# Optimization experiments

Hardware: AMD Instinct MI355X
Metric: run time of the kernel (lower is better)

Reference implementation:

```python
import jax, jax.numpy as jnp
import numpy as np

DIM = 1024
DEPTH = 8
HEADS = 16
DIM_HEAD = 64
INNER = HEADS * DIM_HEAD  # 1024
NQ = 64
EMB = 768
OUT = 1024
FF_INNER = 4 * DIM
B, N1 = 32, 257
EPS = 1e-5


def layer_norm(x, g, b):
    m = jnp.mean(x, axis=-1, keepdims=True)
    v = jnp.mean(jnp.square(x - m), axis=-1, keepdims=True)
    return (x - m) * jax.lax.rsqrt(v + EPS) * g + b


def split_heads(t):
    # (b, l, inner) -> (b, h, l, dh)
    b, l, _ = t.shape
    return t.reshape(b, l, HEADS, DIM_HEAD).transpose(0, 2, 1, 3)


def setup_inputs() -> dict:
    key = jax.random.key(0)
    ks = jax.random.split(key, 12)
    s = 0.02
    inp = {
        "x": jax.random.normal(ks[0], (B, N1, EMB), jnp.float32),
        "latents": jax.random.normal(ks[1], (1, NQ, DIM), jnp.float32) / np.sqrt(DIM),
        "proj_in_w": jax.random.normal(ks[2], (EMB, DIM), jnp.float32) * s,
        "proj_in_b": jnp.zeros((DIM,), jnp.float32),
        "ln1_g": jnp.ones((DEPTH, DIM), jnp.float32),
        "ln1_b": jnp.zeros((DEPTH, DIM), jnp.float32),
        "ln2_g": jnp.ones((DEPTH, DIM), jnp.float32),
        "ln2_b": jnp.zeros((DEPTH, DIM), jnp.float32),
        "Wq": jax.random.normal(ks[3], (DEPTH, DIM, INNER), jnp.float32) * s,
        "Wkv": jax.random.normal(ks[4], (DEPTH, DIM, 2 * INNER), jnp.float32) * s,
        "Wo": jax.random.normal(ks[5], (DEPTH, INNER, DIM), jnp.float32) * s,
        "ff_ln_g": jnp.ones((DEPTH, DIM), jnp.float32),
        "ff_ln_b": jnp.zeros((DEPTH, DIM), jnp.float32),
        "ff_w1": jax.random.normal(ks[6], (DEPTH, DIM, FF_INNER), jnp.float32) * s,
        "ff_w2": jax.random.normal(ks[7], (DEPTH, FF_INNER, DIM), jnp.float32) * s,
        "proj_out_w": jax.random.uniform(ks[8], (DIM, OUT), jnp.float32, -0.01, 0.01),
        "proj_out_b": jnp.zeros((OUT,), jnp.float32),
        "norm_out_g": jnp.ones((OUT,), jnp.float32),
        "norm_out_b": jnp.zeros((OUT,), jnp.float32),
    }
    return inp


def reference(x, latents, proj_in_w, proj_in_b, ln1_g, ln1_b, ln2_g, ln2_b,
              Wq, Wkv, Wo, ff_ln_g, ff_ln_b, ff_w1, ff_w2,
              proj_out_w, proj_out_b, norm_out_g, norm_out_b):
    # proj_in
    xf = x @ proj_in_w + proj_in_b              # (b, n1, dim)
    lat = jnp.broadcast_to(latents, (x.shape[0], NQ, DIM))
    scale = DIM_HEAD ** -0.25                   # 1/sqrt(sqrt(dim_head))

    for i in range(DEPTH):
        # PerceiverAttention
        xn = layer_norm(xf, ln1_g[i], ln1_b[i])
        ln_lat = layer_norm(lat, ln2_g[i], ln2_b[i])
        q = split_heads(ln_lat @ Wq[i])                       # (b,h,nq,dh)
        kv = jnp.concatenate([xn, ln_lat], axis=1) @ Wkv[i]   # (b,n1+nq,2*inner)
        k, v = jnp.split(kv, 2, axis=-1)
        k, v = split_heads(k), split_heads(v)                 # (b,h,nk,dh)
        w = jnp.einsum('bhqd,bhkd->bhqk', q * scale, k * scale)
        w = jax.nn.softmax(w.astype(jnp.float32), axis=-1).astype(q.dtype)
        o = jnp.einsum('bhqk,bhkd->bhqd', w, v)               # (b,h,nq,dh)
        o = o.transpose(0, 2, 1, 3).reshape(lat.shape[0], NQ, INNER)
        lat = o @ Wo[i] + lat
        # FeedForward: LN -> Linear -> GELU -> Linear
        h = layer_norm(lat, ff_ln_g[i], ff_ln_b[i])
        h = jax.nn.gelu(h @ ff_w1[i], approximate=False) @ ff_w2[i]
        lat = h + lat

    out = lat @ proj_out_w + proj_out_b
    return layer_norm(out, norm_out_g, norm_out_b)
```

## Files before the change

### kernel.cpp

```cpp
#include <hip/hip_runtime.h>
#include <hip/hip_bf16.h>
#include <cstdint>

typedef __hip_bfloat16 bf16;
typedef __attribute__((ext_vector_type(8))) short short8;
typedef __attribute__((ext_vector_type(4))) float f32x4;

__device__ __forceinline__ f32x4 mfma16(short8 a, short8 b, f32x4 c) {
  return __builtin_amdgcn_mfma_f32_16x16x32_bf16(a, b, c, 0, 0, 0);
}

__device__ __forceinline__ void gload16(const bf16* g, bf16* l) {
  __builtin_amdgcn_global_load_lds((const __attribute__((address_space(1))) void*)g,
                                   (__attribute__((address_space(3))) void*)l, 16, 0, 0);
}


__global__ void __launch_bounds__(256) cvt_f32_bf16(const float* __restrict__ in,
                                                    bf16* __restrict__ out, int n) {
  int i = blockIdx.x * 256 + threadIdx.x;
  if (i < n) out[i] = __float2bfloat16(in[i]);
}


__device__ __forceinline__ void trans_tile(float (*tile)[33], const float* __restrict__ src,
                                           bf16* __restrict__ dst, int K, int N,
                                           int bx, int by) {
  int n0 = bx * 32, k0 = by * 32;
  int tx = threadIdx.x & 31, ty = threadIdx.x >> 5;
#pragma unroll
  for (int j = 0; j < 32; j += 8)
    tile[ty + j][tx] = src[(size_t)(k0 + ty + j) * N + n0 + tx];
  __syncthreads();
#pragma unroll
  for (int j = 0; j < 32; j += 8)
    dst[(size_t)(n0 + ty + j) * K + k0 + tx] = __float2bfloat16(tile[tx][ty + j]);
}

__global__ void __launch_bounds__(256) transpose_cvt(const float* __restrict__ src,
                                                     bf16* __restrict__ dst,
                                                     int K, int N) {
  __shared__ float tile[32][33];
  trans_tile(tile, src, dst, K, N, blockIdx.x, blockIdx.y);
}

__global__ void __launch_bounds__(256) transpose_all(
    const float* __restrict__ wq, const float* __restrict__ wkv,
    const float* __restrict__ wo, const float* __restrict__ w1,
    const float* __restrict__ w2, bf16* __restrict__ wq_t, bf16* __restrict__ wkv_t,
    bf16* __restrict__ wo_t, bf16* __restrict__ w1_t, bf16* __restrict__ w2_t) {
  __shared__ float tile[32][33];
  int id = blockIdx.x;
  if (id < 1024) {
    trans_tile(tile, wq, wq_t, 1024, 1024, id & 31, id >> 5);
  } else if (id < 3072) {
    id -= 1024;
    trans_tile(tile, wkv, wkv_t, 1024, 2048, id & 63, id >> 6);
  } else if (id < 4096) {
    id -= 3072;
    trans_tile(tile, wo, wo_t, 1024, 1024, id & 31, id >> 5);
  } else if (id < 8192) {
    id -= 4096;
    trans_tile(tile, w1, w1_t, 1024, 4096, id & 127, id >> 7);
  } else {
    id -= 8192;
    trans_tile(tile, w2, w2_t, 4096, 1024, id & 31, id >> 5);
  }
}


__device__ __forceinline__ void stats_of(const float v[4], int tid, float& mean,
                                         float& rstd, float* red) {
  float s = 0.f, s2 = 0.f;
#pragma unroll
  for (int j = 0; j < 4; j++) { s += v[j]; s2 += v[j] * v[j]; }
#pragma unroll
  for (int o = 32; o > 0; o >>= 1) {
    s += __shfl_down(s, o);
    s2 += __shfl_down(s2, o);
  }
  int w = tid >> 6;
  if ((tid & 63) == 0) { red[w] = s; red[4 + w] = s2; }
  __syncthreads();
  s = red[0] + red[1] + red[2] + red[3];
  s2 = red[4] + red[5] + red[6] + red[7];
  mean = s * (1.f / 1024.f);
  float var = s2 * (1.f / 1024.f) - mean * mean;
  rstd = rsqrtf(var + 1e-5f);
}

__device__ __forceinline__ void row_stats(const float* x, int tid, float v[4],
                                          float& mean, float& rstd, float* red) {
#pragma unroll
  for (int j = 0; j < 4; j++) v[j] = x[tid + j * 256];
  stats_of(v, tid, mean, rstd, red);
}

__global__ void __launch_bounds__(256) ln_to_bf16(const float* __restrict__ in,
                                                  const float* __restrict__ g,
                                                  const float* __restrict__ bb,
                                                  bf16* __restrict__ out) {
  __shared__ float red[8];
  int row = blockIdx.x, tid = threadIdx.x;
  const float* x = in + (size_t)row * 1024;
  float v[4], mean, rstd;
  row_stats(x, tid, v, mean, rstd, red);
  bf16* o1 = out + (size_t)row * 1024;
#pragma unroll
  for (int j = 0; j < 4; j++) {
    int c = tid + j * 256;
    float y = (v[j] - mean) * rstd;
    if (g) y = y * g[c] + bb[c];
    o1[c] = __float2bfloat16(y);
  }
}

template <int LM>
__global__ void __launch_bounds__(256) lncat(const bf16* __restrict__ xhat,
                                             const float* __restrict__ lin,
                                             const float* __restrict__ parts,
                                             const float* __restrict__ lat2,
                                             float* __restrict__ lat,
                                             const float* __restrict__ g1,
                                             const float* __restrict__ b1,
                                             const float* __restrict__ g2,
                                             const float* __restrict__ b2,
                                             bf16* __restrict__ cat,
                                             bf16* __restrict__ lnlat) {
  __shared__ float red[8];
  int row = blockIdx.x, tid = threadIdx.x;
  int bidx = row / 336, n = row - bidx * 336;
  bf16* out = cat + (size_t)row * 1024;
  const size_t MN = (size_t)2048 * 1024;
  if (n < 257) {
    const bf16* in = xhat + ((size_t)bidx * 257 + n) * 1024;
#pragma unroll
    for (int j = 0; j < 4; j++) {
      int c = tid + j * 256;
      out[c] = __float2bfloat16(__bfloat162float(in[c]) * g1[c] + b1[c]);
    }
  } else if (n < 321) {
    int lrow = bidx * 64 + (n - 257);
    float v[4];
#pragma unroll
    for (int j = 0; j < 4; j++) {
      int c = tid + j * 256;
      size_t idx = (size_t)lrow * 1024 + c;
      float a;
      if (LM == 0) {
        a = lin[(size_t)(n - 257) * 1024 + c];
      } else {
        a = parts[idx] + parts[MN + idx] + parts[2 * MN + idx] + parts[3 * MN + idx]
          + lat2[idx];
      }
      lat[idx] = a;
      v[j] = a;
    }
    float mean, rstd;
    stats_of(v, tid, mean, rstd, red);
    bf16* o2 = lnlat + (size_t)lrow * 1024;
#pragma unroll
    for (int j = 0; j < 4; j++) {
      int c = tid + j * 256;
      bf16 hh = __float2bfloat16((v[j] - mean) * rstd * g2[c] + b2[c]);
      out[c] = hh;
      o2[c] = hh;
    }
  } else {
#pragma unroll
    for (int j = 0; j < 4; j++)
      out[tid + j * 256] = __float2bfloat16(0.f);
  }
}


enum { MB_BIAS = 1, MB_RESID = 2, MB_GELU = 4, MB_BF16 = 8 };

template <int MODE>
__device__ __forceinline__ void gemm_tile(
    const bf16* __restrict__ A, const bf16* __restrict__ Bt, void* __restrict__ Cout,
    const float* __restrict__ bias, const float* __restrict__ resid,
    int M, int N, int K, int m0, int n0, int kBeg, int kEnd, size_t planeOff,
    bf16* sA, bf16* sB) {
  int tid = threadIdx.x;
  int wave = tid >> 6, lane = tid & 63;
  int quad = lane >> 4, l16 = lane & 15;
  int wm = (wave >> 1) * 64, wn = (wave & 1) * 64;

  int srow = wave * 16 + (lane >> 2);
  int scol = (lane & 3) * 8;
  const bf16* gA0 = A + (size_t)min(m0 + srow, M - 1) * K + scol;
  const bf16* gA1 = A + (size_t)min(m0 + 64 + srow, M - 1) * K + scol;
  const bf16* gB0 = Bt + (size_t)(n0 + srow) * K + scol;
  const bf16* gB1 = Bt + (size_t)(n0 + 64 + srow) * K + scol;
  bf16* lA0 = &sA[(wave * 16) * 32];
  bf16* lA1 = &sA[(64 + wave * 16) * 32];
  bf16* lB0 = &sB[(wave * 16) * 32];
  bf16* lB1 = &sB[(64 + wave * 16) * 32];

  f32x4 acc[4][4] = {};

  for (int k0 = kBeg; k0 < kEnd; k0 += 32) {
    gload16(gA0 + k0, lA0);
    gload16(gA1 + k0, lA1);
    gload16(gB0 + k0, lB0);
    gload16(gB1 + k0, lB1);
    __syncthreads();
    short8 af[4], bfv[4];
#pragma unroll
    for (int i = 0; i < 4; i++)
      af[i] = *(const short8*)&sA[(wm + i * 16 + l16) * 32 + quad * 8];
#pragma unroll
    for (int j = 0; j < 4; j++)
      bfv[j] = *(const short8*)&sB[(wn + j * 16 + l16) * 32 + quad * 8];
#pragma unroll
    for (int i = 0; i < 4; i++)
#pragma unroll
      for (int j = 0; j < 4; j++)
        acc[i][j] = mfma16(af[i], bfv[j], acc[i][j]);
    __syncthreads();
  }

  float* cf = (float*)Cout + planeOff;
#pragma unroll
  for (int i = 0; i < 4; i++) {
    int grb = m0 + wm + i * 16 + quad * 4;
#pragma unroll
    for (int j = 0; j < 4; j++) {
      int gc = n0 + wn + j * 16 + l16;
      float bv = (MODE & MB_BIAS) ? bias[gc] : 0.f;
#pragma unroll
      for (int r = 0; r < 4; r++) {
        int gr = grb + r;
        if (gr < M) {
          float vv = acc[i][j][r] + bv;
          if (MODE & MB_GELU) vv = 0.5f * vv * (1.f + erff(vv * 0.70710678118654752f));
          if (MODE & MB_RESID) vv += resid[(size_t)gr * N + gc];
          if (MODE & MB_BF16) ((bf16*)Cout)[(size_t)gr * N + gc] = __float2bfloat16(vv);
          else cf[(size_t)gr * N + gc] = vv;
        }
      }
    }
  }
}

template <int MODE>
__global__ void __launch_bounds__(256, 2) gemm_bt(
    const bf16* __restrict__ A, const bf16* __restrict__ Bt,
    void* __restrict__ Cout, const float* __restrict__ bias,
    const float* __restrict__ resid, int M, int N, int K) {
  __shared__ bf16 sA[128 * 32];
  __shared__ bf16 sB[128 * 32];
  int kPer = K / gridDim.z;
  gemm_tile<MODE>(A, Bt, Cout, bias, resid, M, N, K,
                  blockIdx.y * 128, blockIdx.x * 128,
                  blockIdx.z * kPer, (blockIdx.z + 1) * kPer,
                  (size_t)blockIdx.z * ((size_t)M * N), sA, sB);
}

__global__ void __launch_bounds__(256, 2) gemm_qkv(
    const bf16* __restrict__ catb, const bf16* __restrict__ wkv,
    bf16* __restrict__ kvbuf, const bf16* __restrict__ lnlat,
    const bf16* __restrict__ wq, bf16* __restrict__ qbuf) {
  __shared__ bf16 sA[128 * 32];
  __shared__ bf16 sB[128 * 32];
  int by = blockIdx.y, bx = blockIdx.x;
  if (by < 84) {
    gemm_tile<MB_BF16>(catb, wkv, kvbuf, nullptr, nullptr, 10752, 2048, 1024,
                       by * 128, bx * 128, 0, 1024, 0, sA, sB);
  } else {
    int t = (by - 84) * 16 + bx;
    gemm_tile<MB_BF16>(lnlat, wq, qbuf, nullptr, nullptr, 2048, 1024, 1024,
                       (t >> 3) * 128, (t & 7) * 128, 0, 1024, 0, sA, sB);
  }
}


enum { RD_BIAS = 1, RD_RESID = 2, RD_BF16 = 4 };

template <int MODE>
__global__ void __launch_bounds__(256) reduce_k(const float* __restrict__ parts, int S,
                                                int MN, int N,
                                                const float* __restrict__ bias,
                                                const float* __restrict__ resid,
                                                void* __restrict__ out) {
  int i4 = (blockIdx.x * 256 + threadIdx.x) * 4;
  if (i4 >= MN) return;
  float4 a = *(const float4*)&parts[i4];
#pragma unroll 4
  for (int s = 1; s < S; s++) {
    float4 b = *(const float4*)&parts[(size_t)s * MN + i4];
    a.x += b.x; a.y += b.y; a.z += b.z; a.w += b.w;
  }
  if (MODE & RD_BIAS) {
    float4 b = *(const float4*)&bias[i4 & (N - 1)];
    a.x += b.x; a.y += b.y; a.z += b.z; a.w += b.w;
  }
  if (MODE & RD_RESID) {
    float4 b = *(const float4*)&resid[i4];
    a.x += b.x; a.y += b.y; a.z += b.z; a.w += b.w;
  }
  if (MODE & RD_BF16) {
    bf16 o[4] = {__float2bfloat16(a.x), __float2bfloat16(a.y),
                 __float2bfloat16(a.z), __float2bfloat16(a.w)};
    *(uint2*)&((bf16*)out)[i4] = *(uint2*)o;
  } else {
    *(float4*)&((float*)out)[i4] = a;
  }
}

__global__ void __launch_bounds__(256) reduce_ln_resid(
    const float* __restrict__ parts, const float* __restrict__ resid,
    const float* __restrict__ g, const float* __restrict__ bb,
    float* __restrict__ lat2, bf16* __restrict__ lnff) {
  __shared__ float red[8];
  int row = blockIdx.x, tid = threadIdx.x;
  const size_t MN = (size_t)2048 * 1024;
  float v[4];
#pragma unroll
  for (int j = 0; j < 4; j++) {
    int c = tid + j * 256;
    size_t idx = (size_t)row * 1024 + c;
    float a = parts[idx] + parts[MN + idx] + parts[2 * MN + idx] + parts[3 * MN + idx]
            + resid[idx];
    lat2[idx] = a;
    v[j] = a;
  }
  float mean, rstd;
  stats_of(v, tid, mean, rstd, red);
  bf16* o = lnff + (size_t)row * 1024;
#pragma unroll
  for (int j = 0; j < 4; j++) {
    int c = tid + j * 256;
    o[c] = __float2bfloat16((v[j] - mean) * rstd * g[c] + bb[c]);
  }
}

__global__ void __launch_bounds__(256) reduce_bias_ln(
    const float* __restrict__ parts, const float* __restrict__ bias,
    const float* __restrict__ g, const float* __restrict__ bb,
    float* __restrict__ out) {
  __shared__ float red[8];
  int row = blockIdx.x, tid = threadIdx.x;
  const size_t MN = (size_t)2048 * 1024;
  float v[4];
#pragma unroll
  for (int j = 0; j < 4; j++) {
    int c = tid + j * 256;
    size_t idx = (size_t)row * 1024 + c;
    v[j] = parts[idx] + parts[MN + idx] + parts[2 * MN + idx] + parts[3 * MN + idx]
         + bias[c];
  }
  float mean, rstd;
  stats_of(v, tid, mean, rstd, red);
  float* o = out + (size_t)row * 1024;
#pragma unroll
  for (int j = 0; j < 4; j++) {
    int c = tid + j * 256;
    o[c] = (v[j] - mean) * rstd * g[c] + bb[c];
  }
}


__device__ __forceinline__ int swz64(int row, int cb) {
  return (row << 7) + (cb ^ ((row & 7) << 4) ^ (((row >> 3) & 3) << 5));
}

__global__ void __launch_bounds__(256, 2) attn(const bf16* __restrict__ qb,
                                               const bf16* __restrict__ kvb,
                                               bf16* __restrict__ ob) {
  __shared__ bf16 sQ[64 * 64];
  __shared__ bf16 sKV[64 * 64];
  __shared__ bf16 sP[64 * 376];
  __shared__ float sRed[256];
  char* cQ = (char*)sQ;
  char* cKV = (char*)sKV;

  int h = blockIdx.x, b = blockIdx.y;
  int tid = threadIdx.x, wave = tid >> 6, lane = tid & 63;
  int quad = lane >> 4, l16 = lane & 15;

  const bf16* qg = qb + (size_t)b * 64 * 1024 + h * 64;
  const bf16* kg = kvb + (size_t)b * 336 * 2048 + h * 64;
  const bf16* vg = kg + 1024;

  {
    int r = tid >> 3, cb = (tid & 7) * 16;
    *(uint4*)(cQ + swz64(r, cb)) =
        *(const uint4*)((const char*)qg + (size_t)r * 2048 + cb);
    *(uint4*)(cQ + swz64(r + 32, cb)) =
        *(const uint4*)((const char*)qg + (size_t)(r + 32) * 2048 + cb);
  }

  f32x4 accS[6][4] = {};

  for (int g = 0; g < 6; g++) {
    __syncthreads();
    {
      int r = tid >> 3, cb = (tid & 7) * 16;
      int gr = g * 64 + r;
      if (gr < 336)
        *(uint4*)(cKV + swz64(r, cb)) =
            *(const uint4*)((const char*)kg + (size_t)gr * 4096 + cb);
      gr += 32;
      if (gr < 336)
        *(uint4*)(cKV + swz64(r + 32, cb)) =
            *(const uint4*)((const char*)kg + (size_t)gr * 4096 + cb);
    }
    __syncthreads();
    if (g * 4 + wave < 21) {
#pragma unroll
      for (int ks = 0; ks < 2; ks++) {
        short8 bfr = *(const short8*)(cKV + swz64(wave * 16 + l16, ks * 64 + quad * 16));
#pragma unroll
        for (int i = 0; i < 4; i++) {
          short8 afr = *(const short8*)(cQ + swz64(i * 16 + l16, ks * 64 + quad * 16));
          accS[g][i] = mfma16(afr, bfr, accS[g][i]);
        }
      }
    }
  }

  float rmax[4][4], rsum[4][4];
#pragma unroll
  for (int i = 0; i < 4; i++)
#pragma unroll
    for (int r = 0; r < 4; r++) { rmax[i][r] = -1e30f; rsum[i][r] = 0.f; }

#pragma unroll
  for (int g = 0; g < 6; g++) {
    int col = (g * 4 + wave) * 16 + l16;
    bool valid = col < 321;
#pragma unroll
    for (int i = 0; i < 4; i++)
#pragma unroll
      for (int r = 0; r < 4; r++) {
        float v = accS[g][i][r] * 0.125f;
        accS[g][i][r] = v;
        if (valid) rmax[i][r] = fmaxf(rmax[i][r], v);
      }
  }
#pragma unroll
  for (int off = 1; off < 16; off <<= 1)
#pragma unroll
    for (int i = 0; i < 4; i++)
#pragma unroll
      for (int r = 0; r < 4; r++)
        rmax[i][r] = fmaxf(rmax[i][r], __shfl_xor(rmax[i][r], off));
  if (l16 == 0) {
#pragma unroll
    for (int i = 0; i < 4; i++)
#pragma unroll
      for (int r = 0; r < 4; r++)
        sRed[wave * 64 + i * 16 + quad * 4 + r] = rmax[i][r];
  }
  __syncthreads();
#pragma unroll
  for (int i = 0; i < 4; i++)
#pragma unroll
    for (int r = 0; r < 4; r++) {
      int row = i * 16 + quad * 4 + r;
      rmax[i][r] = fmaxf(fmaxf(sRed[row], sRed[64 + row]),
                         fmaxf(sRed[128 + row], sRed[192 + row]));
    }
  __syncthreads();

#pragma unroll
  for (int g = 0; g < 6; g++) {
    int col = (g * 4 + wave) * 16 + l16;
    bool valid = col < 321;
#pragma unroll
    for (int i = 0; i < 4; i++)
#pragma unroll
      for (int r = 0; r < 4; r++) {
        float pv = valid ? __expf(accS[g][i][r] - rmax[i][r]) : 0.f;
        rsum[i][r] += pv;
        if (col < 352) sP[(i * 16 + quad * 4 + r) * 376 + col] = __float2bfloat16(pv);
      }
  }
#pragma unroll
  for (int off = 1; off < 16; off <<= 1)
#pragma unroll
    for (int i = 0; i < 4; i++)
#pragma unroll
      for (int r = 0; r < 4; r++)
        rsum[i][r] += __shfl_xor(rsum[i][r], off);
  if (l16 == 0) {
#pragma unroll
    for (int i = 0; i < 4; i++)
#pragma unroll
      for (int r = 0; r < 4; r++)
        sRed[wave * 64 + i * 16 + quad * 4 + r] = rsum[i][r];
  }
  __syncthreads();
#pragma unroll
  for (int i = 0; i < 4; i++)
#pragma unroll
    for (int r = 0; r < 4; r++) {
      int row = i * 16 + quad * 4 + r;
      rsum[i][r] = sRed[row] + sRed[64 + row] + sRed[128 + row] + sRed[192 + row];
    }

  f32x4 accO[4] = {};
  for (int cch = 0; cch < 6; cch++) {
    __syncthreads();
    {
      int r = tid >> 3, cb = (tid & 7) * 16;
      int gr = cch * 64 + r;
      if (gr < 336)
        *(uint4*)(cKV + swz64(r, cb)) =
            *(const uint4*)((const char*)vg + (size_t)gr * 4096 + cb);
      gr += 32;
      if (gr < 336)
        *(uint4*)(cKV + swz64(r + 32, cb)) =
            *(const uint4*)((const char*)vg + (size_t)gr * 4096 + cb);
    }
    __syncthreads();
    int nks = (cch == 5) ? 1 : 2;
    for (int ks = 0; ks < nks; ks++) {
      short8 bv;
      int cb = (wave * 16 + l16) * 2;
#pragma unroll
      for (int jj = 0; jj < 8; jj++)
        bv[jj] = *(const short*)(cKV + swz64(ks * 32 + quad * 8 + jj, cb));
#pragma unroll
      for (int i = 0; i < 4; i++) {
        short8 ap = *(const short8*)&sP[(i * 16 + l16) * 376 + cch * 64 + ks * 32 + quad * 8];
        accO[i] = mfma16(ap, bv, accO[i]);
      }
    }
  }

#pragma unroll
  for (int i = 0; i < 4; i++)
#pragma unroll
    for (int r = 0; r < 4; r++) {
      int row = i * 16 + quad * 4 + r;
      ob[(size_t)(b * 64 + row) * 1024 + h * 64 + wave * 16 + l16] =
          __float2bfloat16(accO[i][r] / rsum[i][r]);
    }
}


extern "C" void kernel_launch(void* const* d_in, const int* in_sizes, int n_in,
                              void* d_out, int out_size, void* d_ws, size_t ws_size,
                              hipStream_t stream) {
  (void)in_sizes; (void)n_in; (void)out_size; (void)ws_size;
  const float* x    = (const float*)d_in[0];
  const float* lin  = (const float*)d_in[1];
  const float* piw  = (const float*)d_in[2];
  const float* pib  = (const float*)d_in[3];
  const float* ln1g = (const float*)d_in[4];
  const float* ln1b = (const float*)d_in[5];
  const float* ln2g = (const float*)d_in[6];
  const float* ln2b = (const float*)d_in[7];
  const float* Wq   = (const float*)d_in[8];
  const float* Wkv  = (const float*)d_in[9];
  const float* Wo   = (const float*)d_in[10];
  const float* ffg  = (const float*)d_in[11];
  const float* ffb  = (const float*)d_in[12];
  const float* W1   = (const float*)d_in[13];
  const float* W2   = (const float*)d_in[14];
  const float* poW  = (const float*)d_in[15];
  const float* pob  = (const float*)d_in[16];
  const float* nog  = (const float*)d_in[17];
  const float* nob  = (const float*)d_in[18];

  char* p = (char*)d_ws;
  auto alloc = [&](size_t bytes) -> char* {
    char* q = p; p += (bytes + 255) & ~(size_t)255; return q;
  };
  bf16* pin_t  = (bf16*)alloc((size_t)1024 * 768 * 2);
  bf16* pout_t = (bf16*)alloc((size_t)1024 * 1024 * 2);
  bf16* wq_t   = (bf16*)alloc((size_t)1024 * 1024 * 2);
  bf16* wkv_t  = (bf16*)alloc((size_t)2048 * 1024 * 2);
  bf16* wo_t   = (bf16*)alloc((size_t)1024 * 1024 * 2);
  bf16* w1_t   = (bf16*)alloc((size_t)4096 * 1024 * 2);
  bf16* w2_t   = (bf16*)alloc((size_t)1024 * 4096 * 2);
  bf16* x_bf   = (bf16*)alloc((size_t)8224 * 768 * 2);
  float* xf    = (float*)alloc((size_t)8224 * 1024 * 4);
  bf16* xhat   = (bf16*)alloc((size_t)8224 * 1024 * 2);
  bf16* cat    = (bf16*)alloc((size_t)10752 * 1024 * 2);
  bf16* lnlat  = (bf16*)alloc((size_t)2048 * 1024 * 2);
  bf16* qbuf   = (bf16*)alloc((size_t)2048 * 1024 * 2);
  bf16* kvbuf  = (bf16*)alloc((size_t)10752 * 2048 * 2);
  bf16* obuf   = (bf16*)alloc((size_t)2048 * 1024 * 2);
  float* lat   = (float*)alloc((size_t)2048 * 1024 * 4);
  float* lat2  = (float*)alloc((size_t)2048 * 1024 * 4);
  bf16* lnff   = (bf16*)alloc((size_t)2048 * 1024 * 2);
  bf16* h1     = (bf16*)alloc((size_t)2048 * 4096 * 2);

  const int MN = 2048 * 1024;

  cvt_f32_bf16<<<6316032 / 256, 256, 0, stream>>>(x, x_bf, 6316032);
  transpose_cvt<<<dim3(32, 24), 256, 0, stream>>>(piw, pin_t, 768, 1024);
  transpose_cvt<<<dim3(32, 32), 256, 0, stream>>>(poW, pout_t, 1024, 1024);
  gemm_bt<MB_BIAS><<<dim3(8, 65), 256, 0, stream>>>(x_bf, pin_t, xf, pib, nullptr,
                                                    8224, 1024, 768);
  ln_to_bf16<<<8224, 256, 0, stream>>>(xf, nullptr, nullptr, xhat);

  for (int i = 0; i < 8; i++) {
    transpose_all<<<12288, 256, 0, stream>>>(
        Wq + (size_t)i * 1048576, Wkv + (size_t)i * 2097152, Wo + (size_t)i * 1048576,
        W1 + (size_t)i * 4194304, W2 + (size_t)i * 4194304,
        wq_t, wkv_t, wo_t, w1_t, w2_t);
    if (i == 0)
      lncat<0><<<10752, 256, 0, stream>>>(xhat, lin, nullptr, nullptr, lat,
                                          ln1g + i * 1024, ln1b + i * 1024,
                                          ln2g + i * 1024, ln2b + i * 1024, cat, lnlat);
    else
      lncat<1><<<10752, 256, 0, stream>>>(xhat, nullptr, xf, lat2, lat,
                                          ln1g + i * 1024, ln1b + i * 1024,
                                          ln2g + i * 1024, ln2b + i * 1024, cat, lnlat);
    gemm_qkv<<<dim3(16, 92), 256, 0, stream>>>(cat, wkv_t, kvbuf, lnlat, wq_t, qbuf);
    attn<<<dim3(16, 32), 256, 0, stream>>>(qbuf, kvbuf, obuf);
    gemm_bt<0><<<dim3(8, 16, 4), 256, 0, stream>>>(obuf, wo_t, xf, nullptr, nullptr,
                                                   2048, 1024, 1024);
    reduce_ln_resid<<<2048, 256, 0, stream>>>(xf, lat, ffg + i * 1024, ffb + i * 1024,
                                              lat2, lnff);
    gemm_bt<MB_GELU | MB_BF16><<<dim3(32, 16), 256, 0, stream>>>(lnff, w1_t, h1, nullptr,
                                                                 nullptr, 2048, 4096, 1024);
    gemm_bt<0><<<dim3(8, 16, 4), 256, 0, stream>>>(h1, w2_t, xf, nullptr, nullptr,
                                                   2048, 1024, 4096);
    if (i == 7)
      reduce_k<RD_RESID | RD_BF16><<<MN / 1024, 256, 0, stream>>>(
          xf, 4, MN, 1024, nullptr, lat2, lnff);
  }

  gemm_bt<0><<<dim3(8, 16, 4), 256, 0, stream>>>(lnff, pout_t, xf, nullptr, nullptr,
                                                 2048, 1024, 1024);
  reduce_bias_ln<<<2048, 256, 0, stream>>>(xf, pob, nog, nob, (float*)d_out);
}
```

Baseline: 2.000 ms.

## Vectorize elementwise kernels, widen GEMM K-tile to 64, halve split-K

Rewrites the conversion, transpose, layernorm and reduction kernels to use float4 loads and packed bf16 stores, with 64x64 transpose tiles. The GEMM tile now stages 64 K-elements per iteration instead of 32, so there are half as many barriers per K step at the cost of doubled LDS. Split-K for the Wo, W2 and output projection GEMMs drops from 4 to 2 partial planes, and the reductions are updated to sum only two planes. This lowers reduction traffic but leaves fewer blocks per GEMM launch.

Result: slower. 2.086 ms (+4.3%).

```diff
diff --git a/kernel.cpp b/kernel.cpp
--- a/kernel.cpp
+++ b/kernel.cpp
@@ -17,31 +17,46 @@
 
 
 __global__ void __launch_bounds__(256) cvt_f32_bf16(const float* __restrict__ in,
-                                                    bf16* __restrict__ out, int n) {
+                                                    bf16* __restrict__ out, int n4) {
   int i = blockIdx.x * 256 + threadIdx.x;
-  if (i < n) out[i] = __float2bfloat16(in[i]);
-}
-
-
-__device__ __forceinline__ void trans_tile(float (*tile)[33], const float* __restrict__ src,
-                                           bf16* __restrict__ dst, int K, int N,
-                                           int bx, int by) {
-  int n0 = bx * 32, k0 = by * 32;
-  int tx = threadIdx.x & 31, ty = threadIdx.x >> 5;
-#pragma unroll
-  for (int j = 0; j < 32; j += 8)
-    tile[ty + j][tx] = src[(size_t)(k0 + ty + j) * N + n0 + tx];
+  if (i < n4) {
+    float4 v = *(const float4*)&in[(size_t)i * 4];
+    bf16 o[4] = {__float2bfloat16(v.x), __float2bfloat16(v.y),
+                 __float2bfloat16(v.z), __float2bfloat16(v.w)};
+    *(uint2*)&out[(size_t)i * 4] = *(uint2*)o;
+  }
+}
+
+
+__device__ __forceinline__ void trans_tile64(float (*t)[65], const float* __restrict__ src,
+                                             bf16* __restrict__ dst, int K, int N,
+                                             int bx, int by) {
+  int n0 = bx * 64, k0 = by * 64;
+  int tx = threadIdx.x & 15, ty = threadIdx.x >> 4;
+#pragma unroll
+  for (int j = 0; j < 64; j += 16) {
+    float4 v = *(const float4*)&src[(size_t)(k0 + ty + j) * N + n0 + tx * 4];
+    t[ty + j][tx * 4 + 0] = v.x;
+    t[ty + j][tx * 4 + 1] = v.y;
+    t[ty + j][tx * 4 + 2] = v.z;
+    t[ty + j][tx * 4 + 3] = v.w;
+  }
   __syncthreads();
-#pragma unroll
-  for (int j = 0; j < 32; j += 8)
-    dst[(size_t)(n0 + ty + j) * K + k0 + tx] = __float2bfloat16(tile[tx][ty + j]);
+  int cb = tx * 4;
+#pragma unroll
+  for (int jj = 0; jj < 4; jj++) {
+    int r = ty + jj * 16;
+    bf16 o[4] = {__float2bfloat16(t[cb + 0][r]), __float2bfloat16(t[cb + 1][r]),
+                 __float2bfloat16(t[cb + 2][r]), __float2bfloat16(t[cb + 3][r])};
+    *(uint2*)&dst[(size_t)(n0 + r) * K + k0 + cb] = *(uint2*)o;
+  }
 }
 
 __global__ void __launch_bounds__(256) transpose_cvt(const float* __restrict__ src,
                                                      bf16* __restrict__ dst,
                                                      int K, int N) {
-  __shared__ float tile[32][33];
-  trans_tile(tile, src, dst, K, N, blockIdx.x, blockIdx.y);
+  __shared__ float tile[64][65];
+  trans_tile64(tile, src, dst, K, N, blockIdx.x, blockIdx.y);
 }
 
 __global__ void __launch_bounds__(256) transpose_all(
@@ -49,31 +64,30 @@
     const float* __restrict__ wo, const float* __restrict__ w1,
     const float* __restrict__ w2, bf16* __restrict__ wq_t, bf16* __restrict__ wkv_t,
     bf16* __restrict__ wo_t, bf16* __restrict__ w1_t, bf16* __restrict__ w2_t) {
-  __shared__ float tile[32][33];
+  __shared__ float tile[64][65];
   int id = blockIdx.x;
-  if (id < 1024) {
-    trans_tile(tile, wq, wq_t, 1024, 1024, id & 31, id >> 5);
-  } else if (id < 3072) {
+  if (id < 256) {
+    trans_tile64(tile, wq, wq_t, 1024, 1024, id & 15, id >> 4);
+  } else if (id < 768) {
+    id -= 256;
+    trans_tile64(tile, wkv, wkv_t, 1024, 2048, id & 31, id >> 5);
+  } else if (id < 1024) {
+    id -= 768;
+    trans_tile64(tile, wo, wo_t, 1024, 1024, id & 15, id >> 4);
+  } else if (id < 2048) {
     id -= 1024;
-    trans_tile(tile, wkv, wkv_t, 1024, 2048, id & 63, id >> 6);
-  } else if (id < 4096) {
-    id -= 3072;
-    trans_tile(tile, wo, wo_t, 1024, 1024, id & 31, id >> 5);
-  } else if (id < 8192) {
-    id -= 4096;
-    trans_tile(tile, w1, w1_t, 1024, 4096, id & 127, id >> 7);
+    trans_tile64(tile, w1, w1_t, 1024, 4096, id & 63, id >> 6);
   } else {
-    id -= 8192;
-    trans_tile(tile, w2, w2_t, 4096, 1024, id & 31, id >> 5);
-  }
-}
-
-
-__device__ __forceinline__ void stats_of(const float v[4], int tid, float& mean,
-                                         float& rstd, float* red) {
-  float s = 0.f, s2 = 0.f;
-#pragma unroll
-  for (int j = 0; j < 4; j++) { s += v[j]; s2 += v[j] * v[j]; }
+    id -= 2048;
+    trans_tile64(tile, w2, w2_t, 4096, 1024, id & 15, id >> 4);
+  }
+}
+
+
+__device__ __forceinline__ void stats4(float4 v, int tid, float& mean,
+                                       float& rstd, float* red) {
+  float s = v.x + v.y + v.z + v.w;
+  float s2 = v.x * v.x + v.y * v.y + v.z * v.z + v.w * v.w;
 #pragma unroll
   for (int o = 32; o > 0; o >>= 1) {
     s += __shfl_down(s, o);
@@ -89,11 +103,10 @@
   rstd = rsqrtf(var + 1e-5f);
 }
 
-__device__ __forceinline__ void row_stats(const float* x, int tid, float v[4],
-                                          float& mean, float& rstd, float* red) {
-#pragma unroll
-  for (int j = 0; j < 4; j++) v[j] = x[tid + j * 256];
-  stats_of(v, tid, mean, rstd, red);
+__device__ __forceinline__ void pack4(bf16* dst, float a, float b, float c, float d) {
+  bf16 o[4] = {__float2bfloat16(a), __float2bfloat16(b),
+               __float2bfloat16(c), __float2bfloat16(d)};
+  *(uint2*)dst = *(uint2*)o;
 }
 
 __global__ void __launch_bounds__(256) ln_to_bf16(const float* __restrict__ in,
@@ -101,18 +114,19 @@
                                                   const float* __restrict__ bb,
                                                   bf16* __restrict__ out) {
   __shared__ float red[8];
-  int row = blockIdx.x, tid = threadIdx.x;
-  const float* x = in + (size_t)row * 1024;
-  float v[4], mean, rstd;
-  row_stats(x, tid, v, mean, rstd, red);
-  bf16* o1 = out + (size_t)row * 1024;
-#pragma unroll
-  for (int j = 0; j < 4; j++) {
-    int c = tid + j * 256;
-    float y = (v[j] - mean) * rstd;
-    if (g) y = y * g[c] + bb[c];
-    o1[c] = __float2bfloat16(y);
-  }
+  int row = blockIdx.x, tid = threadIdx.x, c4 = tid * 4;
+  float4 v = *(const float4*)&in[(size_t)row * 1024 + c4];
+  float mean, rstd;
+  stats4(v, tid, mean, rstd, red);
+  float y0 = (v.x - mean) * rstd, y1 = (v.y - mean) * rstd;
+  float y2 = (v.z - mean) * rstd, y3 = (v.w - mean) * rstd;
+  if (g) {
+    float4 gv = *(const float4*)&g[c4];
+    float4 bv = *(const float4*)&bb[c4];
+    y0 = y0 * gv.x + bv.x; y1 = y1 * gv.y + bv.y;
+    y2 = y2 * gv.z + bv.z; y3 = y3 * gv.w + bv.w;
+  }
+  pack4(&out[(size_t)row * 1024 + c4], y0, y1, y2, y3);
 }
 
 template <int LM>
@@ -128,48 +142,47 @@
                                              bf16* __restrict__ cat,
                                              bf16* __restrict__ lnlat) {
   __shared__ float red[8];
-  int row = blockIdx.x, tid = threadIdx.x;
+  int row = blockIdx.x, tid = threadIdx.x, c4 = tid * 4;
   int bidx = row / 336, n = row - bidx * 336;
   bf16* out = cat + (size_t)row * 1024;
   const size_t MN = (size_t)2048 * 1024;
   if (n < 257) {
     const bf16* in = xhat + ((size_t)bidx * 257 + n) * 1024;
-#pragma unroll
-    for (int j = 0; j < 4; j++) {
-      int c = tid + j * 256;
-      out[c] = __float2bfloat16(__bfloat162float(in[c]) * g1[c] + b1[c]);
-    }
+    uint2 rw = *(const uint2*)&in[c4];
+    const bf16* rb = (const bf16*)&rw;
+    float4 gv = *(const float4*)&g1[c4];
+    float4 bv = *(const float4*)&b1[c4];
+    pack4(&out[c4], __bfloat162float(rb[0]) * gv.x + bv.x,
+          __bfloat162float(rb[1]) * gv.y + bv.y,
+          __bfloat162float(rb[2]) * gv.z + bv.z,
+          __bfloat162float(rb[3]) * gv.w + bv.w);
   } else if (n < 321) {
     int lrow = bidx * 64 + (n - 257);
-    float v[4];
-#pragma unroll
-    for (int j = 0; j < 4; j++) {
-      int c = tid + j * 256;
-      size_t idx = (size_t)lrow * 1024 + c;
-      float a;
-      if (LM == 0) {
-        a = lin[(size_t)(n - 257) * 1024 + c];
-      } else {
-        a = parts[idx] + parts[MN + idx] + parts[2 * MN + idx] + parts[3 * MN + idx]
-          + lat2[idx];
-      }
-      lat[idx] = a;
-      v[j] = a;
-    }
+    size_t idx = (size_t)lrow * 1024 + c4;
+    float4 a;
+    if (LM == 0) {
+      a = *(const float4*)&lin[(size_t)(n - 257) * 1024 + c4];
+    } else {
+      float4 p0 = *(const float4*)&parts[idx];
+      float4 p1 = *(const float4*)&parts[MN + idx];
+      float4 r2 = *(const float4*)&lat2[idx];
+      a.x = p0.x + p1.x + r2.x; a.y = p0.y + p1.y + r2.y;
+      a.z = p0.z + p1.z + r2.z; a.w = p0.w + p1.w + r2.w;
+    }
+    *(float4*)&lat[idx] = a;
     float mean, rstd;
-    stats_of(v, tid, mean, rstd, red);
-    bf16* o2 = lnlat + (size_t)lrow * 1024;
-#pragma unroll
-    for (int j = 0; j < 4; j++) {
-      int c = tid + j * 256;
-      bf16 hh = __float2bfloat16((v[j] - mean) * rstd * g2[c] + b2[c]);
-      out[c] = hh;
-      o2[c] = hh;
-    }
+    stats4(a, tid, mean, rstd, red);
+    float4 gv = *(const float4*)&g2[c4];
+    float4 bv = *(const float4*)&b2[c4];
+    bf16 o[4] = {__float2bfloat16((a.x - mean) * rstd * gv.x + bv.x),
+                 __float2bfloat16((a.y - mean) * rstd * gv.y + bv.y),
+                 __float2bfloat16((a.z - mean) * rstd * gv.z + bv.z),
+                 __float2bfloat16((a.w - mean) * rstd * gv.w + bv.w)};
+    *(uint2*)&out[c4] = *(uint2*)o;
+    *(uint2*)&lnlat[idx] = *(uint2*)o;
   } else {
-#pragma unroll
-    for (int j = 0; j < 4; j++)
-      out[tid + j * 256] = __float2bfloat16(0.f);
+    uint2 z = {0, 0};
+    *(uint2*)&out[c4] = z;
   }
 }
 
@@ -187,37 +200,44 @@
   int quad = lane >> 4, l16 = lane & 15;
   int wm = (wave >> 1) * 64, wn = (wave & 1) * 64;
 
-  int srow = wave * 16 + (lane >> 2);
-  int scol = (lane & 3) * 8;
-  const bf16* gA0 = A + (size_t)min(m0 + srow, M - 1) * K + scol;
-  const bf16* gA1 = A + (size_t)min(m0 + 64 + srow, M - 1) * K + scol;
-  const bf16* gB0 = Bt + (size_t)(n0 + srow) * K + scol;
-  const bf16* gB1 = Bt + (size_t)(n0 + 64 + srow) * K + scol;
-  bf16* lA0 = &sA[(wave * 16) * 32];
-  bf16* lA1 = &sA[(64 + wave * 16) * 32];
-  bf16* lB0 = &sB[(wave * 16) * 32];
-  bf16* lB1 = &sB[(64 + wave * 16) * 32];
+  int srow = wave * 8 + (lane >> 3);
+  int scol = (lane & 7) * 8;
+  const bf16* gA[4];
+  const bf16* gB[4];
+#pragma unroll
+  for (int s = 0; s < 4; s++) {
+    gA[s] = A + (size_t)min(m0 + s * 32 + srow, M - 1) * K + scol;
+    gB[s] = Bt + (size_t)(n0 + s * 32 + srow) * K + scol;
+  }
+  bf16* lA = &sA[(wave * 8) * 64];
+  bf16* lB = &sB[(wave * 8) * 64];
 
   f32x4 acc[4][4] = {};
 
-  for (int k0 = kBeg; k0 < kEnd; k0 += 32) {
-    gload16(gA0 + k0, lA0);
-    gload16(gA1 + k0, lA1);
-    gload16(gB0 + k0, lB0);
-    gload16(gB1 + k0, lB1);
+  for (int k0 = kBeg; k0 < kEnd; k0 += 64) {
+#pragma unroll
+    for (int s = 0; s < 4; s++) {
+      gload16(gA[s] + k0, lA + s * 32 * 64);
+      gload16(gB[s] + k0, lB + s * 32 * 64);
+    }
     __syncthreads();
-    short8 af[4], bfv[4];
-#pragma unroll
-    for (int i = 0; i < 4; i++)
-      af[i] = *(const short8*)&sA[(wm + i * 16 + l16) * 32 + quad * 8];
-#pragma unroll
-    for (int j = 0; j < 4; j++)
-      bfv[j] = *(const short8*)&sB[(wn + j * 16 + l16) * 32 + quad * 8];
-#pragma unroll
-    for (int i = 0; i < 4; i++)
+    short8 af[2][4], bfv[2][4];
+#pragma unroll
+    for (int ks = 0; ks < 2; ks++) {
+#pragma unroll
+      for (int i = 0; i < 4; i++)
+        af[ks][i] = *(const short8*)&sA[(wm + i * 16 + l16) * 64 + ks * 32 + quad * 8];
 #pragma unroll
       for (int j = 0; j < 4; j++)
-        acc[i][j] = mfma16(af[i], bfv[j], acc[i][j]);
+        bfv[ks][j] = *(const short8*)&sB[(wn + j * 16 + l16) * 64 + ks * 32 + quad * 8];
+    }
+#pragma unroll
+    for (int ks = 0; ks < 2; ks++)
+#pragma unroll
+      for (int i = 0; i < 4; i++)
+#pragma unroll
+        for (int j = 0; j < 4; j++)
+          acc[ks ? i : i][j] = mfma16(af[ks][i], bfv[ks][j], acc[i][j]);
     __syncthreads();
   }
 
@@ -249,8 +269,8 @@
     const bf16* __restrict__ A, const bf16* __restrict__ Bt,
     void* __restrict__ Cout, const float* __restrict__ bias,
     const float* __restrict__ resid, int M, int N, int K) {
-  __shared__ bf16 sA[128 * 32];
-  __shared__ bf16 sB[128 * 32];
+  __shared__ bf16 sA[128 * 64];
+  __shared__ bf16 sB[128 * 64];
   int kPer = K / gridDim.z;
   gemm_tile<MODE>(A, Bt, Cout, bias, resid, M, N, K,
                   blockIdx.y * 128, blockIdx.x * 128,
@@ -262,8 +282,8 @@
     const bf16* __restrict__ catb, const bf16* __restrict__ wkv,
     bf16* __restrict__ kvbuf, const bf16* __restrict__ lnlat,
     const bf16* __restrict__ wq, bf16* __restrict__ qbuf) {
-  __shared__ bf16 sA[128 * 32];
-  __shared__ bf16 sB[128 * 32];
+  __shared__ bf16 sA[128 * 64];
+  __shared__ bf16 sB[128 * 64];
   int by = blockIdx.y, bx = blockIdx.x;
   if (by < 84) {
     gemm_tile<MB_BF16>(catb, wkv, kvbuf, nullptr, nullptr, 10752, 2048, 1024,
@@ -314,26 +334,24 @@
     const float* __restrict__ g, const float* __restrict__ bb,
     float* __restrict__ lat2, bf16* __restrict__ lnff) {
   __shared__ float red[8];
-  int row = blockIdx.x, tid = threadIdx.x;
+  int row = blockIdx.x, tid = threadIdx.x, c4 = tid * 4;
   const size_t MN = (size_t)2048 * 1024;
-  float v[4];
-#pragma unroll
-  for (int j = 0; j < 4; j++) {
-    int c = tid + j * 256;
-    size_t idx = (size_t)row * 1024 + c;
-    float a = parts[idx] + parts[MN + idx] + parts[2 * MN + idx] + parts[3 * MN + idx]
-            + resid[idx];
-    lat2[idx] = a;
-    v[j] = a;
-  }
+  size_t idx = (size_t)row * 1024 + c4;
+  float4 p0 = *(const float4*)&parts[idx];
+  float4 p1 = *(const float4*)&parts[MN + idx];
+  float4 r2 = *(const float4*)&resid[idx];
+  float4 a;
+  a.x = p0.x + p1.x + r2.x; a.y = p0.y + p1.y + r2.y;
+  a.z = p0.z + p1.z + r2.z; a.w = p0.w + p1.w + r2.w;
+  *(float4*)&lat2[idx] = a;
   float mean, rstd;
-  stats_of(v, tid, mean, rstd, red);
-  bf16* o = lnff + (size_t)row * 1024;
-#pragma unroll
-  for (int j = 0; j < 4; j++) {
-    int c = tid + j * 256;
-    o[c] = __float2bfloat16((v[j] - mean) * rstd * g[c] + bb[c]);
-  }
+  stats4(a, tid, mean, rstd, red);
+  float4 gv = *(const float4*)&g[c4];
+  float4 bv = *(const float4*)&bb[c4];
+  pack4(&lnff[idx], (a.x - mean) * rstd * gv.x + bv.x,
+        (a.y - mean) * rstd * gv.y + bv.y,
+        (a.z - mean) * rstd * gv.z + bv.z,
+        (a.w - mean) * rstd * gv.w + bv.w);
 }
 
 __global__ void __launch_bounds__(256) reduce_bias_ln(
@@ -341,24 +359,25 @@
     const float* __restrict__ g, const float* __restrict__ bb,
     float* __restrict__ out) {
   __shared__ float red[8];
-  int row = blockIdx.x, tid = threadIdx.x;
+  int row = blockIdx.x, tid = threadIdx.x, c4 = tid * 4;
   const size_t MN = (size_t)2048 * 1024;
-  float v[4];
-#pragma unroll
-  for (int j = 0; j < 4; j++) {
-    int c = tid + j * 256;
-    size_t idx = (size_t)row * 1024 + c;
-    v[j] = parts[idx] + parts[MN + idx] + parts[2 * MN + idx] + parts[3 * MN + idx]
-         + bias[c];
-  }
+  size_t idx = (size_t)row * 1024 + c4;
+  float4 p0 = *(const float4*)&parts[idx];
+  float4 p1 = *(const float4*)&parts[MN + idx];
+  float4 bv = *(const float4*)&bias[c4];
+  float4 a;
+  a.x = p0.x + p1.x + bv.x; a.y = p0.y + p1.y + bv.y;
+  a.z = p0.z + p1.z + bv.z; a.w = p0.w + p1.w + bv.w;
   float mean, rstd;
-  stats_of(v, tid, mean, rstd, red);
-  float* o = out + (size_t)row * 1024;
-#pragma unroll
-  for (int j = 0; j < 4; j++) {
-    int c = tid + j * 256;
-    o[c] = (v[j] - mean) * rstd * g[c] + bb[c];
-  }
+  stats4(a, tid, mean, rstd, red);
+  float4 gv = *(const float4*)&g[c4];
+  float4 b2 = *(const float4*)&bb[c4];
+  float4 o;
+  o.x = (a.x - mean) * rstd * gv.x + b2.x;
+  o.y = (a.y - mean) * rstd * gv.y + b2.y;
+  o.z = (a.z - mean) * rstd * gv.z + b2.z;
+  o.w = (a.w - mean) * rstd * gv.w + b2.w;
+  *(float4*)&out[idx] = o;
 }
 
 
@@ -592,15 +611,15 @@
 
   const int MN = 2048 * 1024;
 
-  cvt_f32_bf16<<<6316032 / 256, 256, 0, stream>>>(x, x_bf, 6316032);
-  transpose_cvt<<<dim3(32, 24), 256, 0, stream>>>(piw, pin_t, 768, 1024);
-  transpose_cvt<<<dim3(32, 32), 256, 0, stream>>>(poW, pout_t, 1024, 1024);
+  cvt_f32_bf16<<<(6316032 / 4 + 255) / 256, 256, 0, stream>>>(x, x_bf, 6316032 / 4);
+  transpose_cvt<<<dim3(16, 12), 256, 0, stream>>>(piw, pin_t, 768, 1024);
+  transpose_cvt<<<dim3(16, 16), 256, 0, stream>>>(poW, pout_t, 1024, 1024);
   gemm_bt<MB_BIAS><<<dim3(8, 65), 256, 0, stream>>>(x_bf, pin_t, xf, pib, nullptr,
                                                     8224, 1024, 768);
   ln_to_bf16<<<8224, 256, 0, stream>>>(xf, nullptr, nullptr, xhat);
 
   for (int i = 0; i < 8; i++) {
-    transpose_all<<<12288, 256, 0, stream>>>(
+    transpose_all<<<3072, 256, 0, stream>>>(
         Wq + (size_t)i * 1048576, Wkv + (size_t)i * 2097152, Wo + (size_t)i * 1048576,
         W1 + (size_t)i * 4194304, W2 + (size_t)i * 4194304,
         wq_t, wkv_t, wo_t, w1_t, w2_t);
@@ -614,20 +633,20 @@
                                           ln2g + i * 1024, ln2b + i * 1024, cat, lnlat);
     gemm_qkv<<<dim3(16, 92), 256, 0, stream>>>(cat, wkv_t, kvbuf, lnlat, wq_t, qbuf);
     attn<<<dim3(16, 32), 256, 0, stream>>>(qbuf, kvbuf, obuf);
-    gemm_bt<0><<<dim3(8, 16, 4), 256, 0, stream>>>(obuf, wo_t, xf, nullptr, nullptr,
+    gemm_bt<0><<<dim3(8, 16, 2), 256, 0, stream>>>(obuf, wo_t, xf, nullptr, nullptr,
                                                    2048, 1024, 1024);
     reduce_ln_resid<<<2048, 256, 0, stream>>>(xf, lat, ffg + i * 1024, ffb + i * 1024,
                                               lat2, lnff);
     gemm_bt<MB_GELU | MB_BF16><<<dim3(32, 16), 256, 0, stream>>>(lnff, w1_t, h1, nullptr,
                                                                  nullptr, 2048, 4096, 1024);
-    gemm_bt<0><<<dim3(8, 16, 4), 256, 0, stream>>>(h1, w2_t, xf, nullptr, nullptr,
+    gemm_bt<0><<<dim3(8, 16, 2), 256, 0, stream>>>(h1, w2_t, xf, nullptr, nullptr,
                                                    2048, 1024, 4096);
     if (i == 7)
       reduce_k<RD_RESID | RD_BF16><<<MN / 1024, 256, 0, stream>>>(
-          xf, 4, MN, 1024, nullptr, lat2, lnff);
-  }
-
-  gemm_bt<0><<<dim3(8, 16, 4), 256, 0, stream>>>(lnff, pout_t, xf, nullptr, nullptr,
+          xf, 2, MN, 1024, nullptr, lat2, lnff);
+  }
+
+  gemm_bt<0><<<dim3(8, 16, 2), 256, 0, stream>>>(lnff, pout_t, xf, nullptr, nullptr,
                                                  2048, 1024, 1024);
   reduce_bias_ln<<<2048, 256, 0, stream>>>(xf, pob, nog, nob, (float*)d_out);
 }
```
